# Kernel optimization log

Measured on AMD Instinct MI355X. Metric: run time of the kernel, lower is better.

## Reference

```python
import jax, jax.numpy as jnp
import numpy as np
import math

D_MODEL = 2048
NUM_HEADS = 16
HEAD_DIM = D_MODEL // NUM_HEADS
B, QLEN, CACHE_LEN = 4, 512, 3584

def setup_inputs() -> dict:
    key = jax.random.key(0)
    ks = jax.random.split(key, 13)
    s = 0.02
    return {
        'query': jax.random.normal(ks[0], (B, QLEN, D_MODEL), jnp.float32),
        'key': jax.random.normal(ks[1], (B, QLEN, D_MODEL), jnp.float32),
        'value': jax.random.normal(ks[2], (B, QLEN, D_MODEL), jnp.float32),
        'cached_k': jax.random.normal(ks[3], (B, CACHE_LEN, D_MODEL), jnp.float32),
        'cached_v': jax.random.normal(ks[4], (B, CACHE_LEN, D_MODEL), jnp.float32),
        'wq': jax.random.normal(ks[5], (D_MODEL, D_MODEL), jnp.float32) * s,
        'bq': jnp.zeros((D_MODEL,), jnp.float32),
        'wk': jax.random.normal(ks[6], (D_MODEL, D_MODEL), jnp.float32) * s,
        'bk': jnp.zeros((D_MODEL,), jnp.float32),
        'wv': jax.random.normal(ks[7], (D_MODEL, D_MODEL), jnp.float32) * s,
        'bv': jnp.zeros((D_MODEL,), jnp.float32),
        'wo': jax.random.normal(ks[8], (D_MODEL, D_MODEL), jnp.float32) * s,
        'bo': jnp.zeros((D_MODEL,), jnp.float32),
    }

def _split_heads(x):
    b, s, _ = x.shape
    return x.reshape(b, s, NUM_HEADS, HEAD_DIM).transpose(0, 2, 1, 3)  # [b,h,s,d]

def reference(query, key, value, cached_k, cached_v, wq, bq, wk, bk, wv, bv, wo, bo):
    # projections (torch Linear: x @ W^T + b)
    Q = query @ wq.T + bq
    K_new = key @ wk.T + bk
    V_new = value @ wv.T + bv
    K = jnp.concatenate([cached_k, K_new], axis=1)  # [b, total, d_model]
    V = jnp.concatenate([cached_v, V_new], axis=1)
    seq_len = query.shape[1]
    total_len = K.shape[1]
    cache_len = total_len - seq_len
    Qh = _split_heads(Q)  # [b,h,q,d]
    Kh = _split_heads(K)  # [b,h,t,d]
    Vh = _split_heads(V)
    scale = math.sqrt(HEAD_DIM)
    scores = jnp.einsum('bhqd,bhtd->bhqt', Qh, Kh) / scale
    # causal mask with cache offset: query i attends to keys j <= cache_len + i
    q_idx = jnp.arange(seq_len)[:, None]
    k_idx = jnp.arange(total_len)[None, :]
    mask = k_idx > (q_idx + cache_len)  # True = masked
    scores = jnp.where(mask[None, None], -jnp.inf, scores)
    attn = jax.nn.softmax(scores, axis=-1)
    out = jnp.einsum('bhqt,bhtd->bhqd', attn, Vh)
    out = out.transpose(0, 2, 1, 3).reshape(query.shape[0], seq_len, D_MODEL)
    out = out @ wo.T + bo
    return out
```

## Files before the change

kernel.cpp:

```cpp
#include <hip/hip_runtime.h>

typedef _Float16 half8 __attribute__((ext_vector_type(8)));
typedef _Float16 half4v __attribute__((ext_vector_type(4)));
typedef float f32x4 __attribute__((ext_vector_type(4)));

#define NB 4
#define SQ 512
#define CL 3584
#define TT 4096
#define DM 2048
#define NH 16
#define DH 128

#define KSW(row, col) ((((row) * 128) + (col)) ^ ((((row) & 7) << 3)))
#define VSW(row, col) ((((row) * 64) + (col)) ^ ((((row) & 7) << 3)))
#define PSW(row, col) ((((row) * 64) + (col)) ^ ((((row) & 7) << 3)))

__device__ __forceinline__ void gl_lds16(const void* g, void* l) {
  __builtin_amdgcn_global_load_lds(
      (const __attribute__((address_space(1))) unsigned int*)g,
      (__attribute__((address_space(3))) unsigned int*)l, 16, 0, 0);
}

__global__ __launch_bounds__(256) void cvt_f16(
    const float* __restrict__ s0, const float* __restrict__ s1, const float* __restrict__ s2,
    const float* __restrict__ s3, const float* __restrict__ s4, const float* __restrict__ s5,
    _Float16* __restrict__ d0, _Float16* __restrict__ d1, _Float16* __restrict__ d2,
    _Float16* __restrict__ d3, _Float16* __restrict__ d4, _Float16* __restrict__ d5)
{
  const int z = blockIdx.y;
  const float* s = z == 0 ? s0 : z == 1 ? s1 : z == 2 ? s2 : z == 3 ? s3 : z == 4 ? s4 : s5;
  _Float16* d = z == 0 ? d0 : z == 1 ? d1 : z == 2 ? d2 : z == 3 ? d3 : z == 4 ? d4 : d5;
  const int n4 = DM * DM / 4;
  for (int v = blockIdx.x * blockDim.x + threadIdx.x; v < n4;
       v += gridDim.x * blockDim.x) {
    float4 x = ((const float4*)s)[v];
    half4v h = { (_Float16)x.x, (_Float16)x.y, (_Float16)x.z, (_Float16)x.w };
    ((half4v*)d)[v] = h;
  }
}

__global__ __launch_bounds__(256) void cvt_f16_one(
    const float* __restrict__ s, _Float16* __restrict__ d)
{
  const int n4 = DM * DM / 4;
  for (int v = blockIdx.x * blockDim.x + threadIdx.x; v < n4;
       v += gridDim.x * blockDim.x) {
    float4 x = ((const float4*)s)[v];
    half4v h = { (_Float16)x.x, (_Float16)x.y, (_Float16)x.z, (_Float16)x.w };
    ((half4v*)d)[v] = h;
  }
}

__global__ __launch_bounds__(256) void convert_K(
    const float* __restrict__ ck, _Float16* __restrict__ K)
{
  const long long nvec = (long long)NB * CL * DM / 4;
  const int pb = CL * DM / 4;
  for (long long v = (long long)blockIdx.x * blockDim.x + threadIdx.x; v < nvec;
       v += (long long)gridDim.x * blockDim.x) {
    int b = (int)(v / pb);
    long long r = v - (long long)b * pb;
    float4 x = ((const float4*)ck)[v];
    half4v hx = { (_Float16)x.x, (_Float16)x.y, (_Float16)x.z, (_Float16)x.w };
    ((half4v*)K)[(long long)b * (TT * DM / 4) + r] = hx;
  }
}

__global__ __launch_bounds__(512) void fused_pre(
    const _Float16* __restrict__ A0, const _Float16* __restrict__ A1,
    const _Float16* __restrict__ A2,
    const _Float16* __restrict__ W0, const _Float16* __restrict__ W1,
    const _Float16* __restrict__ W2,
    const float* __restrict__ b0, const float* __restrict__ b1,
    const float* __restrict__ b2,
    _Float16* __restrict__ Qp, _Float16* __restrict__ Kc,
    _Float16* __restrict__ Vt, const float* __restrict__ cv)
{
  __shared__ __align__(16) char smem[4 * 8192];

  const int bid = blockIdx.x;
  const int tid = threadIdx.x;

  if (bid < 768) {
    char* Abuf = smem;
    char* Wbuf = smem + 2 * 8192;
    const int bm = bid & 15, bn = (bid >> 4) & 15, z = bid >> 8;
    const _Float16* Ain = z == 0 ? A0 : z == 1 ? A1 : A2;
    const _Float16* W   = z == 0 ? W0 : z == 1 ? W1 : W2;
    const float* bias   = z == 0 ? b0 : z == 1 ? b1 : b2;

    const int wid = tid >> 6, lane = tid & 63;
    const int wm = wid >> 2, wn = wid & 3;
    const int lr = lane & 15, lg = lane >> 4;

    f32x4 acc[4][2];
#pragma unroll
    for (int i = 0; i < 4; ++i)
#pragma unroll
      for (int j = 0; j < 2; ++j) acc[i][j] = (f32x4){0.f, 0.f, 0.f, 0.f};

    size_t aoff, woff;
    {
      const int o = wid * 1024 + lane * 16;
      const int prow = o >> 7, pb = o & 127;
      const int lb = pb ^ ((prow & 7) << 4);
      const int r = (prow << 1) | (lb >> 6), c = lb & 63;
      aoff = (size_t)(bm * 128 + r) * 4096 + c;
      woff = (size_t)(bn * 128 + r) * 4096 + c;
    }

    auto stage = [&](int kt, int buf) {
      gl_lds16((const char*)Ain + aoff + kt * 64, Abuf + buf * 8192 + wid * 1024);
      gl_lds16((const char*)W + woff + kt * 64, Wbuf + buf * 8192 + wid * 1024);
    };
    auto lds_addr = [](const char* base, int r, int cb) -> const char* {
      return base + ((r >> 1) << 7) + ((((r & 1) << 6) | cb) ^ (((r >> 1) & 7) << 4));
    };
    auto compute = [&](int buf) {
      const char* ab = Abuf + buf * 8192;
      const char* wb = Wbuf + buf * 8192;
      half8 af[4], bf[2];
#pragma unroll
      for (int i = 0; i < 4; ++i)
        af[i] = *(const half8*)lds_addr(ab, wm * 64 + i * 16 + lr, lg << 4);
#pragma unroll
      for (int j = 0; j < 2; ++j)
        bf[j] = *(const half8*)lds_addr(wb, wn * 32 + j * 16 + lr, lg << 4);
#pragma unroll
      for (int i = 0; i < 4; ++i)
#pragma unroll
        for (int j = 0; j < 2; ++j)
          acc[i][j] = __builtin_amdgcn_mfma_f32_16x16x32_f16(af[i], bf[j], acc[i][j], 0, 0, 0);
    };

    const int NKT = DM / 32;
    stage(0, 0);
    __syncthreads();
    for (int kt = 0; kt < NKT; ++kt) {
      if (kt + 1 < NKT) stage(kt + 1, (kt + 1) & 1);
      compute(kt & 1);
      __syncthreads();
    }

    const float qscale = 0.08838834764831845f * 1.4426950408889634f;
#pragma unroll
    for (int i = 0; i < 4; ++i) {
      const int m0 = bm * 128 + wm * 64 + i * 16 + lg * 4;
#pragma unroll
      for (int j = 0; j < 2; ++j) {
        const int gn = bn * 128 + wn * 32 + j * 16 + lr;
        const float bb = bias[gn];
        if (z == 0) {
#pragma unroll
          for (int r = 0; r < 4; ++r)
            Qp[(size_t)(m0 + r) * DM + gn] = (_Float16)((acc[i][j][r] + bb) * qscale);
        } else if (z == 1) {
          const int b = m0 >> 9;
#pragma unroll
          for (int r = 0; r < 4; ++r)
            Kc[((size_t)b * TT + CL + ((m0 + r) & 511)) * DM + gn] =
                (_Float16)(acc[i][j][r] + bb);
        } else {
          half4v hv;
#pragma unroll
          for (int r = 0; r < 4; ++r) hv[r] = (_Float16)(acc[i][j][r] + bb);
          const int b = m0 >> 9, t = CL + (m0 & 511);
          const int h = gn >> 7, d = gn & 127;
          *(half4v*)&Vt[((size_t)(b * NH + h) * DH + d) * TT + t] = hv;
        }
      }
    }
  } else {
    _Float16 (*T)[136] = (_Float16(*)[136])smem;
    const int tv = bid - 768;
    const int b = tv / 896;
    const int rem = tv - b * 896;
    const int t0 = (rem % 56) * 64;
    const int dm0 = (rem / 56) * 128;
    {
      const int tr = tid >> 3, c0 = (tid & 7) * 16;
      const float* src = cv + ((size_t)b * CL + t0 + tr) * DM + dm0 + c0;
      float4 a0 = ((const float4*)src)[0];
      float4 a1 = ((const float4*)src)[1];
      float4 a2 = ((const float4*)src)[2];
      float4 a3 = ((const float4*)src)[3];
      half8 h0 = { (_Float16)a0.x, (_Float16)a0.y, (_Float16)a0.z, (_Float16)a0.w,
                   (_Float16)a1.x, (_Float16)a1.y, (_Float16)a1.z, (_Float16)a1.w };
      half8 h1 = { (_Float16)a2.x, (_Float16)a2.y, (_Float16)a2.z, (_Float16)a2.w,
                   (_Float16)a3.x, (_Float16)a3.y, (_Float16)a3.z, (_Float16)a3.w };
      *(half8*)&T[tr][c0] = h0;
      *(half8*)&T[tr][c0 + 8] = h1;
    }
    __syncthreads();
    {
      const int dl = tid >> 2, tc = (tid & 3) * 16;
      const int h = dm0 >> 7;
      half8 o0, o1;
#pragma unroll
      for (int i = 0; i < 8; ++i) o0[i] = T[tc + i][dl];
#pragma unroll
      for (int i = 0; i < 8; ++i) o1[i] = T[tc + 8 + i][dl];
      _Float16* dst = Vt + ((size_t)(b * NH + h) * DH + dl) * TT + t0 + tc;
      *(half8*)dst = o0;
      *(half8*)(dst + 8) = o1;
    }
  }
}

__global__ __launch_bounds__(512, 4) void mm16o(
    const _Float16* __restrict__ Ain, const _Float16* __restrict__ W,
    const float* __restrict__ bias, float* __restrict__ Co)
{
  __shared__ __align__(16) char smem[4 * 8192];
  char* Abuf = smem;
  char* Wbuf = smem + 2 * 8192;

  const int tid = threadIdx.x;
  const int bm = blockIdx.x, bn = blockIdx.y;
  const int wid = tid >> 6, lane = tid & 63;
  const int wm = wid >> 2, wn = wid & 3;
  const int lr = lane & 15, lg = lane >> 4;

  f32x4 acc[4][2];
#pragma unroll
  for (int i = 0; i < 4; ++i)
#pragma unroll
    for (int j = 0; j < 2; ++j) acc[i][j] = (f32x4){0.f, 0.f, 0.f, 0.f};

  size_t aoff, woff;
  {
    const int o = wid * 1024 + lane * 16;
    const int prow = o >> 7, pb = o & 127;
    const int lb = pb ^ ((prow & 7) << 4);
    const int r = (prow << 1) | (lb >> 6), c = lb & 63;
    aoff = (size_t)(bm * 128 + r) * 4096 + c;
    woff = (size_t)(bn * 128 + r) * 4096 + c;
  }

  auto stage = [&](int kt, int buf) {
    gl_lds16((const char*)Ain + aoff + kt * 64, Abuf + buf * 8192 + wid * 1024);
    gl_lds16((const char*)W + woff + kt * 64, Wbuf + buf * 8192 + wid * 1024);
  };
  auto lds_addr = [](const char* base, int r, int cb) -> const char* {
    return base + ((r >> 1) << 7) + ((((r & 1) << 6) | cb) ^ (((r >> 1) & 7) << 4));
  };
  auto compute = [&](int buf) {
    const char* ab = Abuf + buf * 8192;
    const char* wb = Wbuf + buf * 8192;
    half8 af[4], bf[2];
#pragma unroll
    for (int i = 0; i < 4; ++i)
      af[i] = *(const half8*)lds_addr(ab, wm * 64 + i * 16 + lr, lg << 4);
#pragma unroll
    for (int j = 0; j < 2; ++j)
      bf[j] = *(const half8*)lds_addr(wb, wn * 32 + j * 16 + lr, lg << 4);
#pragma unroll
    for (int i = 0; i < 4; ++i)
#pragma unroll
      for (int j = 0; j < 2; ++j)
        acc[i][j] = __builtin_amdgcn_mfma_f32_16x16x32_f16(af[i], bf[j], acc[i][j], 0, 0, 0);
  };

  const int NKT = DM / 32;
  stage(0, 0);
  __syncthreads();
  for (int kt = 0; kt < NKT; ++kt) {
    if (kt + 1 < NKT) stage(kt + 1, (kt + 1) & 1);
    compute(kt & 1);
    __syncthreads();
  }

#pragma unroll
  for (int i = 0; i < 4; ++i) {
    const int m0 = bm * 128 + wm * 64 + i * 16 + lg * 4;
#pragma unroll
    for (int j = 0; j < 2; ++j) {
      const int gn = bn * 128 + wn * 32 + j * 16 + lr;
      const float bb = bias[gn];
#pragma unroll
      for (int r = 0; r < 4; ++r)
        Co[(size_t)(m0 + r) * DM + gn] = acc[i][j][r] + bb;
    }
  }
}

__global__ __launch_bounds__(512) void attn_kernel(
    const _Float16* __restrict__ Qp, const _Float16* __restrict__ Kc,
    const _Float16* __restrict__ Vt, _Float16* __restrict__ O0,
    _Float16* __restrict__ O1, float2* __restrict__ ml)
{
  __shared__ _Float16 Ks[2][64 * 128];
  __shared__ _Float16 VTs[3][128 * 64];
  __shared__ _Float16 Ps[8][32 * 64];

  const int tid = threadIdx.x;
  const int lin = blockIdx.x;
  const int xcd = lin & 7, slot = lin >> 3;
  const int pair = xcd * 8 + (slot >> 2);
  const int rem = slot & 3;
  const int qb = rem >> 1, part = rem & 1;
  const int b = pair >> 4, h = pair & 15;

  const int wid = tid >> 6, lane = tid & 63;
  const int lr = lane & 15, lg = lane >> 4;
  const int qw = qb * 256 + wid * 32;

  half8 qf[2][4];
#pragma unroll
  for (int qs = 0; qs < 2; ++qs)
#pragma unroll
    for (int kk = 0; kk < 4; ++kk)
      qf[qs][kk] = *(const half8*)&Qp[(size_t)(b * SQ + qw + qs * 16 + lr) * DM +
                                      h * DH + kk * 32 + lg * 8];

  f32x4 zero = {0.f, 0.f, 0.f, 0.f};
  f32x4 acc[8][2];
#pragma unroll
  for (int d = 0; d < 8; ++d)
#pragma unroll
    for (int qs = 0; qs < 2; ++qs) acc[d][qs] = zero;
  float m_run[2] = {-1e30f, -1e30f}, l_run[2] = {0.f, 0.f};

  const int nt_full = (CL + qb * 256 + 256) / 64;
  const int halfn = nt_full >> 1;
  const int tbeg = part ? halfn : 0;
  const int nt = part ? (nt_full - halfn) : halfn;

  int ksrc[2], vsrc[2];
#pragma unroll
  for (int c = 0; c < 2; ++c) {
    const int p = c * 512 + wid * 64 + lane;
    { const int r = p >> 4, pg = p & 15, gc = pg ^ (r & 7);
      ksrc[c] = r * DM + gc * 8; }
    { const int d = p >> 3, pg = p & 7, gt = pg ^ (d & 7);
      vsrc[c] = d * TT + gt * 8; }
  }
  const _Float16* Kb = Kc + (size_t)b * TT * DM + h * DH;
  const _Float16* Vb = Vt + (size_t)(b * NH + h) * DH * TT;

  auto stage = [&](int tt, int kbuf, int vbuf) {
    const int t0 = (tbeg + tt) * 64;
#pragma unroll
    for (int c = 0; c < 2; ++c)
      gl_lds16(Kb + (size_t)t0 * DM + ksrc[c], &Ks[kbuf][(c * 512 + wid * 64) * 8]);
#pragma unroll
    for (int c = 0; c < 2; ++c)
      gl_lds16(Vb + t0 + vsrc[c], &VTs[vbuf][(c * 512 + wid * 64) * 8]);
  };

  auto qk = [&](int kbuf, f32x4 (*s)[2]) {
#pragma unroll
    for (int j = 0; j < 4; ++j)
#pragma unroll
      for (int qs = 0; qs < 2; ++qs) s[j][qs] = zero;
#pragma unroll
    for (int kk = 0; kk < 4; ++kk)
#pragma unroll
      for (int j = 0; j < 4; ++j) {
        half8 kb = *(const half8*)&Ks[kbuf][KSW(j * 16 + lr, kk * 32 + lg * 8)];
        s[j][0] = __builtin_amdgcn_mfma_f32_16x16x32_f16(kb, qf[0][kk], s[j][0], 0, 0, 0);
        s[j][1] = __builtin_amdgcn_mfma_f32_16x16x32_f16(kb, qf[1][kk], s[j][1], 0, 0, 0);
      }
  };

  auto mask_s = [&](int t0, f32x4 (*s)[2]) {
    if (part && t0 + 63 > CL + qw) {
#pragma unroll
      for (int j = 0; j < 4; ++j)
#pragma unroll
        for (int qs = 0; qs < 2; ++qs)
#pragma unroll
          for (int r = 0; r < 4; ++r)
            if (t0 + j * 16 + lg * 4 + r > CL + qw + qs * 16 + lr) s[j][qs][r] = -1e30f;
    }
  };

  auto softmax_step = [&](f32x4 (*s)[2]) {
    float mt[2];
#pragma unroll
    for (int qs = 0; qs < 2; ++qs) {
      float m = s[0][qs][0];
#pragma unroll
      for (int j = 0; j < 4; ++j)
#pragma unroll
        for (int r = 0; r < 4; ++r) m = fmaxf(m, s[j][qs][r]);
      mt[qs] = m;
    }
    if (!__all(mt[0] <= m_run[0] + 10.0f && mt[1] <= m_run[1] + 10.0f)) {
#pragma unroll
      for (int qs = 0; qs < 2; ++qs) {
        float m = fmaxf(mt[qs], __shfl_xor(mt[qs], 16));
        m = fmaxf(m, __shfl_xor(m, 32));
        const float mn = fmaxf(m_run[qs], m);
        const float fsc = exp2f(m_run[qs] - mn);
        m_run[qs] = mn;
        l_run[qs] *= fsc;
#pragma unroll
        for (int d = 0; d < 8; ++d)
#pragma unroll
          for (int r = 0; r < 4; ++r) acc[d][qs][r] *= fsc;
      }
    }
#pragma unroll
    for (int qs = 0; qs < 2; ++qs) {
      float ps = 0.f;
#pragma unroll
      for (int j = 0; j < 4; ++j) {
        float p0 = exp2f(s[j][qs][0] - m_run[qs]);
        float p1 = exp2f(s[j][qs][1] - m_run[qs]);
        float p2 = exp2f(s[j][qs][2] - m_run[qs]);
        float p3 = exp2f(s[j][qs][3] - m_run[qs]);
        ps += (p0 + p1) + (p2 + p3);
        half4v hp = { (_Float16)p0, (_Float16)p1, (_Float16)p2, (_Float16)p3 };
        *(half4v*)&Ps[wid][PSW(qs * 16 + lr, j * 16 + lg * 4)] = hp;
      }
      l_run[qs] += ps;
    }
  };

  auto pv = [&](int vbuf) {
#pragma unroll
    for (int kk = 0; kk < 2; ++kk) {
      half8 pf0 = *(const half8*)&Ps[wid][PSW(lr, kk * 32 + lg * 8)];
      half8 pf1 = *(const half8*)&Ps[wid][PSW(16 + lr, kk * 32 + lg * 8)];
#pragma unroll
      for (int d = 0; d < 8; ++d) {
        half8 vf = *(const half8*)&VTs[vbuf][VSW(d * 16 + lr, kk * 32 + lg * 8)];
        acc[d][0] = __builtin_amdgcn_mfma_f32_16x16x32_f16(vf, pf0, acc[d][0], 0, 0, 0);
        acc[d][1] = __builtin_amdgcn_mfma_f32_16x16x32_f16(vf, pf1, acc[d][1], 0, 0, 0);
      }
    }
  };

  f32x4 sp[4][2], sc[4][2];

  stage(0, 0, 0);
  __syncthreads();
  stage(1, 1, 1);
  qk(0, sp);
  mask_s(tbeg * 64, sp);

  for (int t = 1; t < nt; ++t) {
    __syncthreads();
    if (t + 1 < nt) stage(t + 1, (t + 1) & 1, (t + 1) % 3);
    qk(t & 1, sc);
    softmax_step(sp);
    pv((t - 1) % 3);
    mask_s((tbeg + t) * 64, sc);
#pragma unroll
    for (int j = 0; j < 4; ++j)
#pragma unroll
      for (int qs = 0; qs < 2; ++qs) sp[j][qs] = sc[j][qs];
  }
  softmax_step(sp);
  pv((nt - 1) % 3);

  _Float16* Od = part ? O1 : O0;
#pragma unroll
  for (int qs = 0; qs < 2; ++qs) {
    float lt = l_run[qs] + __shfl_xor(l_run[qs], 16);
    lt += __shfl_xor(lt, 32);
    const float inv = 1.0f / lt;
#pragma unroll
    for (int d = 0; d < 8; ++d) {
      half4v hv;
#pragma unroll
      for (int r = 0; r < 4; ++r) hv[r] = (_Float16)(acc[d][qs][r] * inv);
      *(half4v*)&Od[(size_t)(b * SQ + qw + qs * 16 + lr) * DM + h * DH + d * 16 + lg * 4] = hv;
    }
    if (lg == 0) {
      float2 e; e.x = m_run[qs]; e.y = lt;
      ml[part * (64 * SQ) + ((b * NH + h) * SQ) + qw + qs * 16 + lr] = e;
    }
  }
}

__global__ __launch_bounds__(256) void combine(
    _Float16* __restrict__ AO, const _Float16* __restrict__ O1,
    const float2* __restrict__ ml)
{
  const int idx = blockIdx.x * 256 + threadIdx.x;
  const int row = idx >> 8;
  const int col0 = (idx & 255) * 8;
  const int b = row >> 9, q = row & 511, h = col0 >> 7;
  const float2 e0 = ml[(b * NH + h) * SQ + q];
  const float2 e1 = ml[64 * SQ + (b * NH + h) * SQ + q];
  const float m = fmaxf(e0.x, e1.x);
  float w0 = e0.y * exp2f(e0.x - m);
  float w1 = e1.y * exp2f(e1.x - m);
  const float inv = 1.0f / (w0 + w1);
  w0 *= inv; w1 *= inv;
  const size_t o = (size_t)row * DM + col0;
  half8 a = *(const half8*)&AO[o];
  half8 c = *(const half8*)&O1[o];
  half8 r;
#pragma unroll
  for (int i = 0; i < 8; ++i)
    r[i] = (_Float16)(w0 * (float)a[i] + w1 * (float)c[i]);
  *(half8*)&AO[o] = r;
}

extern "C" void kernel_launch(void* const* d_in, const int* in_sizes, int n_in,
                              void* d_out, int out_size, void* d_ws, size_t ws_size,
                              hipStream_t stream) {
  const float* query = (const float*)d_in[0];
  const float* key   = (const float*)d_in[1];
  const float* value = (const float*)d_in[2];
  const float* ck    = (const float*)d_in[3];
  const float* cv    = (const float*)d_in[4];
  const float* wq = (const float*)d_in[5];
  const float* bq = (const float*)d_in[6];
  const float* wk = (const float*)d_in[7];
  const float* bk = (const float*)d_in[8];
  const float* wv = (const float*)d_in[9];
  const float* bv = (const float*)d_in[10];
  const float* wo = (const float*)d_in[11];
  const float* bo = (const float*)d_in[12];

  char* ws = (char*)d_ws;
  _Float16* Kc = (_Float16*)ws;
  _Float16* Vt = (_Float16*)(ws + 67108864);
  _Float16* Qp = (_Float16*)(ws + 134217728);
  _Float16* AO = (_Float16*)(ws + 142606336);

  _Float16* qh = AO;
  _Float16* kh = (_Float16*)d_out;
  _Float16* vh = (_Float16*)((char*)d_out + 8388608);
  _Float16* wqh = Kc;
  _Float16* wkh = (_Float16*)(ws + 16777216);
  _Float16* wvh = (_Float16*)(ws + 33554432);
  _Float16* woh = Qp;

  _Float16* O1s = (_Float16*)d_out;
  float2* mls = (float2*)((char*)d_out + 8388608);

  cvt_f16<<<dim3(512, 6), 256, 0, stream>>>(
      query, key, value, wq, wk, wv, qh, kh, vh, wqh, wkh, wvh);
  fused_pre<<<768 + 3584, 512, 0, stream>>>(
      qh, kh, vh, wqh, wkh, wvh, bq, bk, bv, Qp, Kc, Vt, cv);
  convert_K<<<2048, 256, 0, stream>>>(ck, Kc);
  attn_kernel<<<256, 512, 0, stream>>>(Qp, Kc, Vt, AO, O1s, mls);
  combine<<<2048, 256, 0, stream>>>(AO, O1s, mls);
  cvt_f16_one<<<512, 256, 0, stream>>>(wo, woh);
  mm16o<<<dim3(16, 16), 512, 0, stream>>>(AO, woh, bo, (float*)d_out);
}
```

Measured before the change: 315.7 us.

## Split attention KV range into four parts with smaller key tiles

Adds an attention kernel that splits each query block's key/value range into four parts instead of two, launching 512 blocks with 32-key tiles, new LDS swizzles and double buffering. A four-way combine kernel merges the partial outputs using the stored max/sum pairs. The aim is better CU occupancy and load balance across the GPU. The cost is extra partial-output traffic, more per-tile synchronisation, and extra workspace; it only runs when the workspace is at least 153 MB, otherwise the old two-way path is used.

```diff
diff --git a/kernel.cpp b/kernel.cpp
--- a/kernel.cpp
+++ b/kernel.cpp
@@ -15,6 +15,8 @@
 #define KSW(row, col) ((((row) * 128) + (col)) ^ ((((row) & 7) << 3)))
 #define VSW(row, col) ((((row) * 64) + (col)) ^ ((((row) & 7) << 3)))
 #define PSW(row, col) ((((row) * 64) + (col)) ^ ((((row) & 7) << 3)))
+#define PSW2(row, col) ((((row) << 5)) + ((col) ^ (((row) & 3) << 3)))
+#define VAD(D, g) ((((D) >> 1) * 64) + ((((((D) & 1) << 2) | (g)) ^ (((D) >> 1) & 7)) << 3))
 
 __device__ __forceinline__ void gl_lds16(const void* g, void* l) {
   __builtin_amdgcn_global_load_lds(
@@ -285,7 +287,214 @@
   }
 }
 
-__global__ __launch_bounds__(512) void attn_kernel(
+__global__ __launch_bounds__(512) void attn_kernel4(
+    const _Float16* __restrict__ Qp, const _Float16* __restrict__ Kc,
+    const _Float16* __restrict__ Vt, _Float16* __restrict__ O0,
+    _Float16* __restrict__ O1, _Float16* __restrict__ O2,
+    _Float16* __restrict__ O3, float2* __restrict__ ml)
+{
+  __shared__ _Float16 Ks[2][32 * 128];
+  __shared__ _Float16 VTs[2][64 * 64];
+  __shared__ _Float16 Ps[8][32 * 32];
+
+  const int tid = threadIdx.x;
+  const int lin = blockIdx.x;
+  const int xcd = lin & 7, slot = lin >> 3;
+  const int pair = xcd * 8 + (slot >> 3);
+  const int rem = slot & 7;
+  const int qb = rem >> 2, part = rem & 3;
+  const int b = pair >> 4, h = pair & 15;
+
+  const int wid = tid >> 6, lane = tid & 63;
+  const int lr = lane & 15, lg = lane >> 4;
+  const int qw = qb * 256 + wid * 32;
+
+  half8 qf[2][4];
+#pragma unroll
+  for (int qs = 0; qs < 2; ++qs)
+#pragma unroll
+    for (int kk = 0; kk < 4; ++kk)
+      qf[qs][kk] = *(const half8*)&Qp[(size_t)(b * SQ + qw + qs * 16 + lr) * DM +
+                                      h * DH + kk * 32 + lg * 8];
+
+  f32x4 zero = {0.f, 0.f, 0.f, 0.f};
+  f32x4 acc[8][2];
+#pragma unroll
+  for (int d = 0; d < 8; ++d)
+#pragma unroll
+    for (int qs = 0; qs < 2; ++qs) acc[d][qs] = zero;
+  float m_run[2] = {-1e30f, -1e30f}, l_run[2] = {0.f, 0.f};
+
+  const int nt_full = (CL + qb * 256 + 256) / 32;
+  const int quarter = nt_full >> 2;
+  const int tbeg = part * quarter;
+  const int nt = quarter;
+
+  int ksrc, vsrc;
+  {
+    const int r = tid >> 4, pg = tid & 15;
+    ksrc = r * DM + (pg ^ (r & 7)) * 8;
+  }
+  {
+    const int line = tid >> 3, slot8 = tid & 7;
+    const int un = slot8 ^ (line & 7);
+    const int d = (line << 1) | (un >> 2), g = un & 3;
+    vsrc = d * TT + g * 8;
+  }
+  const _Float16* Kb = Kc + (size_t)b * TT * DM + h * DH;
+  const _Float16* Vb = Vt + (size_t)(b * NH + h) * DH * TT;
+
+  auto stage = [&](int tt, int buf) {
+    const int t0 = (tbeg + tt) * 32;
+    gl_lds16(Kb + (size_t)t0 * DM + ksrc, &Ks[buf][tid * 8]);
+    gl_lds16(Vb + t0 + vsrc, &VTs[buf][tid * 8]);
+  };
+
+  f32x4 s[2][2];
+
+  stage(0, 0);
+  __syncthreads();
+
+  for (int t = 0; t < nt; ++t) {
+    const int cur = t & 1;
+    if (t + 1 < nt) stage(t + 1, cur ^ 1);
+
+#pragma unroll
+    for (int j = 0; j < 2; ++j)
+#pragma unroll
+      for (int qs = 0; qs < 2; ++qs) s[j][qs] = zero;
+#pragma unroll
+    for (int kk = 0; kk < 4; ++kk)
+#pragma unroll
+      for (int j = 0; j < 2; ++j) {
+        half8 kb = *(const half8*)&Ks[cur][KSW(j * 16 + lr, kk * 32 + lg * 8)];
+        s[j][0] = __builtin_amdgcn_mfma_f32_16x16x32_f16(kb, qf[0][kk], s[j][0], 0, 0, 0);
+        s[j][1] = __builtin_amdgcn_mfma_f32_16x16x32_f16(kb, qf[1][kk], s[j][1], 0, 0, 0);
+      }
+
+    if (part == 3) {
+      const int t0 = (tbeg + t) * 32;
+      if (t0 + 31 > CL + qw) {
+#pragma unroll
+        for (int j = 0; j < 2; ++j)
+#pragma unroll
+          for (int qs = 0; qs < 2; ++qs)
+#pragma unroll
+            for (int r = 0; r < 4; ++r)
+              if (t0 + j * 16 + lg * 4 + r > CL + qw + qs * 16 + lr) s[j][qs][r] = -1e30f;
+      }
+    }
+
+    float mt[2];
+#pragma unroll
+    for (int qs = 0; qs < 2; ++qs) {
+      float m = s[0][qs][0];
+#pragma unroll
+      for (int j = 0; j < 2; ++j)
+#pragma unroll
+        for (int r = 0; r < 4; ++r) m = fmaxf(m, s[j][qs][r]);
+      mt[qs] = m;
+    }
+    if (!__all(mt[0] <= m_run[0] + 10.0f && mt[1] <= m_run[1] + 10.0f)) {
+#pragma unroll
+      for (int qs = 0; qs < 2; ++qs) {
+        float m = fmaxf(mt[qs], __shfl_xor(mt[qs], 16));
+        m = fmaxf(m, __shfl_xor(m, 32));
+        const float mn = fmaxf(m_run[qs], m);
+        const float fsc = exp2f(m_run[qs] - mn);
+        m_run[qs] = mn;
+        l_run[qs] *= fsc;
+#pragma unroll
+        for (int d = 0; d < 8; ++d)
+#pragma unroll
+          for (int r = 0; r < 4; ++r) acc[d][qs][r] *= fsc;
+      }
+    }
+#pragma unroll
+    for (int qs = 0; qs < 2; ++qs) {
+      float ps = 0.f;
+#pragma unroll
+      for (int j = 0; j < 2; ++j) {
+        float p0 = exp2f(s[j][qs][0] - m_run[qs]);
+        float p1 = exp2f(s[j][qs][1] - m_run[qs]);
+        float p2 = exp2f(s[j][qs][2] - m_run[qs]);
+        float p3 = exp2f(s[j][qs][3] - m_run[qs]);
+        ps += (p0 + p1) + (p2 + p3);
+        half4v hp = { (_Float16)p0, (_Float16)p1, (_Float16)p2, (_Float16)p3 };
+        *(half4v*)&Ps[wid][PSW2(qs * 16 + lr, j * 16 + lg * 4)] = hp;
+      }
+      l_run[qs] += ps;
+    }
+
+    {
+      half8 pf0 = *(const half8*)&Ps[wid][PSW2(lr, lg * 8)];
+      half8 pf1 = *(const half8*)&Ps[wid][PSW2(16 + lr, lg * 8)];
+#pragma unroll
+      for (int d = 0; d < 8; ++d) {
+        half8 vf = *(const half8*)&VTs[cur][VAD(d * 16 + lr, lg)];
+        acc[d][0] = __builtin_amdgcn_mfma_f32_16x16x32_f16(vf, pf0, acc[d][0], 0, 0, 0);
+        acc[d][1] = __builtin_amdgcn_mfma_f32_16x16x32_f16(vf, pf1, acc[d][1], 0, 0, 0);
+      }
+    }
+
+    __syncthreads();
+  }
+
+  _Float16* Od = part == 0 ? O0 : part == 1 ? O1 : part == 2 ? O2 : O3;
+#pragma unroll
+  for (int qs = 0; qs < 2; ++qs) {
+    float lt = l_run[qs] + __shfl_xor(l_run[qs], 16);
+    lt += __shfl_xor(lt, 32);
+    const float inv = 1.0f / lt;
+#pragma unroll
+    for (int d = 0; d < 8; ++d) {
+      half4v hv;
+#pragma unroll
+      for (int r = 0; r < 4; ++r) hv[r] = (_Float16)(acc[d][qs][r] * inv);
+      *(half4v*)&Od[(size_t)(b * SQ + qw + qs * 16 + lr) * DM + h * DH + d * 16 + lg * 4] = hv;
+    }
+    if (lg == 0) {
+      float2 e; e.x = m_run[qs]; e.y = lt;
+      ml[part * (64 * SQ) + ((b * NH + h) * SQ) + qw + qs * 16 + lr] = e;
+    }
+  }
+}
+
+__global__ __launch_bounds__(256) void combine4(
+    _Float16* __restrict__ AO, const _Float16* __restrict__ O1,
+    const _Float16* __restrict__ O2, const _Float16* __restrict__ O3,
+    const float2* __restrict__ ml)
+{
+  const int idx = blockIdx.x * 256 + threadIdx.x;
+  const int row = idx >> 8;
+  const int col0 = (idx & 255) * 8;
+  const int b = row >> 9, q = row & 511, h = col0 >> 7;
+  const int base = (b * NH + h) * SQ + q;
+  float2 e0 = ml[base];
+  float2 e1 = ml[64 * SQ + base];
+  float2 e2 = ml[2 * 64 * SQ + base];
+  float2 e3 = ml[3 * 64 * SQ + base];
+  float m = fmaxf(fmaxf(e0.x, e1.x), fmaxf(e2.x, e3.x));
+  float w0 = e0.y * exp2f(e0.x - m);
+  float w1 = e1.y * exp2f(e1.x - m);
+  float w2 = e2.y * exp2f(e2.x - m);
+  float w3 = e3.y * exp2f(e3.x - m);
+  const float inv = 1.0f / (((w0 + w1) + (w2 + w3)));
+  w0 *= inv; w1 *= inv; w2 *= inv; w3 *= inv;
+  const size_t o = (size_t)row * DM + col0;
+  half8 a = *(const half8*)&AO[o];
+  half8 c1 = *(const half8*)&O1[o];
+  half8 c2 = *(const half8*)&O2[o];
+  half8 c3 = *(const half8*)&O3[o];
+  half8 r;
+#pragma unroll
+  for (int i = 0; i < 8; ++i)
+    r[i] = (_Float16)(w0 * (float)a[i] + w1 * (float)c1[i] +
+                      w2 * (float)c2[i] + w3 * (float)c3[i]);
+  *(half8*)&AO[o] = r;
+}
+
+__global__ __launch_bounds__(512) void attn_kernel2(
     const _Float16* __restrict__ Qp, const _Float16* __restrict__ Kc,
     const _Float16* __restrict__ Vt, _Float16* __restrict__ O0,
     _Float16* __restrict__ O1, float2* __restrict__ ml)
@@ -476,7 +685,7 @@
   }
 }
 
-__global__ __launch_bounds__(256) void combine(
+__global__ __launch_bounds__(256) void combine2(
     _Float16* __restrict__ AO, const _Float16* __restrict__ O1,
     const float2* __restrict__ ml)
 {
@@ -532,16 +741,27 @@
   _Float16* wvh = (_Float16*)(ws + 33554432);
   _Float16* woh = Qp;
 
-  _Float16* O1s = (_Float16*)d_out;
-  float2* mls = (float2*)((char*)d_out + 8388608);
-
   cvt_f16<<<dim3(512, 6), 256, 0, stream>>>(
       query, key, value, wq, wk, wv, qh, kh, vh, wqh, wkh, wvh);
   fused_pre<<<768 + 3584, 512, 0, stream>>>(
       qh, kh, vh, wqh, wkh, wvh, bq, bk, bv, Qp, Kc, Vt, cv);
   convert_K<<<2048, 256, 0, stream>>>(ck, Kc);
-  attn_kernel<<<256, 512, 0, stream>>>(Qp, Kc, Vt, AO, O1s, mls);
-  combine<<<2048, 256, 0, stream>>>(AO, O1s, mls);
+
+  const bool big = ws_size >= (size_t)153 * 1024 * 1024;
+  if (big) {
+    _Float16* O1s = (_Float16*)d_out;
+    _Float16* O2s = (_Float16*)((char*)d_out + 8388608);
+    _Float16* O3s = (_Float16*)(ws + 150994944);
+    float2* mls = (float2*)(ws + 159383552);
+    attn_kernel4<<<512, 512, 0, stream>>>(Qp, Kc, Vt, AO, O1s, O2s, O3s, mls);
+    combine4<<<2048, 256, 0, stream>>>(AO, O1s, O2s, O3s, mls);
+  } else {
+    _Float16* O1s = (_Float16*)d_out;
+    float2* mls = (float2*)((char*)d_out + 8388608);
+    attn_kernel2<<<256, 512, 0, stream>>>(Qp, Kc, Vt, AO, O1s, mls);
+    combine2<<<2048, 256, 0, stream>>>(AO, O1s, mls);
+  }
+
   cvt_f16_one<<<512, 256, 0, stream>>>(wo, woh);
   mm16o<<<dim3(16, 16), 512, 0, stream>>>(AO, woh, bo, (float*)d_out);
 }
```

Result: slower. 338.9 us (+7.3%).

## Fuse fp32 weight conversion into QKV GEMM staging and fold K-cache conversion

Applied to the files above, without the earlier changes.

The QKV projection GEMM now reads fp32 weights directly. It converts them to fp16 in registers with packed round-toward-zero conversion and writes them to LDS itself, so the separate pass that converted the three weight matrices is gone. The cached-K conversion kernel is folded into fused_pre as 1024 extra blocks, which removes one launch and lets that work overlap with the GEMM and V-transpose blocks. In exchange, each weight tile is fetched as fp32 by every M-block, doubling the weight bytes read from cache. The W staging also now goes through registers rather than direct global-to-LDS loads, and round-toward-zero changes the weight rounding slightly.

```diff
diff --git a/kernel.cpp b/kernel.cpp
--- a/kernel.cpp
+++ b/kernel.cpp
@@ -24,13 +24,11 @@
 
 __global__ __launch_bounds__(256) void cvt_f16(
     const float* __restrict__ s0, const float* __restrict__ s1, const float* __restrict__ s2,
-    const float* __restrict__ s3, const float* __restrict__ s4, const float* __restrict__ s5,
-    _Float16* __restrict__ d0, _Float16* __restrict__ d1, _Float16* __restrict__ d2,
-    _Float16* __restrict__ d3, _Float16* __restrict__ d4, _Float16* __restrict__ d5)
+    _Float16* __restrict__ d0, _Float16* __restrict__ d1, _Float16* __restrict__ d2)
 {
   const int z = blockIdx.y;
-  const float* s = z == 0 ? s0 : z == 1 ? s1 : z == 2 ? s2 : z == 3 ? s3 : z == 4 ? s4 : s5;
-  _Float16* d = z == 0 ? d0 : z == 1 ? d1 : z == 2 ? d2 : z == 3 ? d3 : z == 4 ? d4 : d5;
+  const float* s = z == 0 ? s0 : z == 1 ? s1 : s2;
+  _Float16* d = z == 0 ? d0 : z == 1 ? d1 : d2;
   const int n4 = DM * DM / 4;
   for (int v = blockIdx.x * blockDim.x + threadIdx.x; v < n4;
        v += gridDim.x * blockDim.x) {
@@ -52,30 +50,16 @@
   }
 }
 
-__global__ __launch_bounds__(256) void convert_K(
-    const float* __restrict__ ck, _Float16* __restrict__ K)
-{
-  const long long nvec = (long long)NB * CL * DM / 4;
-  const int pb = CL * DM / 4;
-  for (long long v = (long long)blockIdx.x * blockDim.x + threadIdx.x; v < nvec;
-       v += (long long)gridDim.x * blockDim.x) {
-    int b = (int)(v / pb);
-    long long r = v - (long long)b * pb;
-    float4 x = ((const float4*)ck)[v];
-    half4v hx = { (_Float16)x.x, (_Float16)x.y, (_Float16)x.z, (_Float16)x.w };
-    ((half4v*)K)[(long long)b * (TT * DM / 4) + r] = hx;
-  }
-}
-
 __global__ __launch_bounds__(512) void fused_pre(
     const _Float16* __restrict__ A0, const _Float16* __restrict__ A1,
     const _Float16* __restrict__ A2,
-    const _Float16* __restrict__ W0, const _Float16* __restrict__ W1,
-    const _Float16* __restrict__ W2,
+    const float* __restrict__ Wq, const float* __restrict__ Wk,
+    const float* __restrict__ Wv,
     const float* __restrict__ b0, const float* __restrict__ b1,
     const float* __restrict__ b2,
     _Float16* __restrict__ Qp, _Float16* __restrict__ Kc,
-    _Float16* __restrict__ Vt, const float* __restrict__ cv)
+    _Float16* __restrict__ Vt, const float* __restrict__ cv,
+    const float* __restrict__ ck)
 {
   __shared__ __align__(16) char smem[4 * 8192];
 
@@ -87,7 +71,7 @@
     char* Wbuf = smem + 2 * 8192;
     const int bm = bid & 15, bn = (bid >> 4) & 15, z = bid >> 8;
     const _Float16* Ain = z == 0 ? A0 : z == 1 ? A1 : A2;
-    const _Float16* W   = z == 0 ? W0 : z == 1 ? W1 : W2;
+    const float* Wf     = z == 0 ? Wq : z == 1 ? Wk : Wv;
     const float* bias   = z == 0 ? b0 : z == 1 ? b1 : b2;
 
     const int wid = tid >> 6, lane = tid & 63;
@@ -100,19 +84,31 @@
 #pragma unroll
       for (int j = 0; j < 2; ++j) acc[i][j] = (f32x4){0.f, 0.f, 0.f, 0.f};
 
-    size_t aoff, woff;
+    size_t aoff, woff32;
     {
       const int o = wid * 1024 + lane * 16;
       const int prow = o >> 7, pb = o & 127;
       const int lb = pb ^ ((prow & 7) << 4);
       const int r = (prow << 1) | (lb >> 6), c = lb & 63;
       aoff = (size_t)(bm * 128 + r) * 4096 + c;
-      woff = (size_t)(bn * 128 + r) * 4096 + c;
-    }
-
-    auto stage = [&](int kt, int buf) {
-      gl_lds16((const char*)Ain + aoff + kt * 64, Abuf + buf * 8192 + wid * 1024);
-      gl_lds16((const char*)W + woff + kt * 64, Wbuf + buf * 8192 + wid * 1024);
+      woff32 = (size_t)(bn * 128 + r) * 8192 + (size_t)c * 2;
+    }
+    const int ldst = wid * 1024 + lane * 16;
+
+    float4 wr0, wr1;
+    auto stage_load = [&](int kt) {
+      gl_lds16((const char*)Ain + aoff + kt * 64, Abuf + ((kt & 1) * 8192) + ldst);
+      const char* wp = (const char*)Wf + woff32 + (size_t)kt * 128;
+      wr0 = *(const float4*)wp;
+      wr1 = *(const float4*)(wp + 16);
+    };
+    auto stage_write = [&](int buf) {
+      int u0 = __builtin_bit_cast(int, __builtin_amdgcn_cvt_pkrtz(wr0.x, wr0.y));
+      int u1 = __builtin_bit_cast(int, __builtin_amdgcn_cvt_pkrtz(wr0.z, wr0.w));
+      int u2 = __builtin_bit_cast(int, __builtin_amdgcn_cvt_pkrtz(wr1.x, wr1.y));
+      int u3 = __builtin_bit_cast(int, __builtin_amdgcn_cvt_pkrtz(wr1.z, wr1.w));
+      uint4 u = { (unsigned)u0, (unsigned)u1, (unsigned)u2, (unsigned)u3 };
+      *(uint4*)(Wbuf + buf * 8192 + ldst) = u;
     };
     auto lds_addr = [](const char* base, int r, int cb) -> const char* {
       return base + ((r >> 1) << 7) + ((((r & 1) << 6) | cb) ^ (((r >> 1) & 7) << 4));
@@ -135,11 +131,13 @@
     };
 
     const int NKT = DM / 32;
-    stage(0, 0);
+    stage_load(0);
+    stage_write(0);
     __syncthreads();
     for (int kt = 0; kt < NKT; ++kt) {
-      if (kt + 1 < NKT) stage(kt + 1, (kt + 1) & 1);
+      if (kt + 1 < NKT) stage_load(kt + 1);
       compute(kt & 1);
+      if (kt + 1 < NKT) stage_write((kt + 1) & 1);
       __syncthreads();
     }
 
@@ -171,7 +169,7 @@
         }
       }
     }
-  } else {
+  } else if (bid < 768 + 3584) {
     _Float16 (*T)[136] = (_Float16(*)[136])smem;
     const int tv = bid - 768;
     const int b = tv / 896;
@@ -205,6 +203,18 @@
       *(half8*)dst = o0;
       *(half8*)(dst + 8) = o1;
     }
+  } else {
+    const int cb = bid - (768 + 3584);
+    const long long nvec = (long long)NB * CL * DM / 4;
+    const int pb = CL * DM / 4;
+    const long long stride = 1024LL * 512;
+    for (long long v = (long long)cb * 512 + tid; v < nvec; v += stride) {
+      int b = (int)(v / pb);
+      long long r = v - (long long)b * pb;
+      float4 x = ((const float4*)ck)[v];
+      half4v hx = { (_Float16)x.x, (_Float16)x.y, (_Float16)x.z, (_Float16)x.w };
+      ((half4v*)Kc)[(long long)b * (TT * DM / 4) + r] = hx;
+    }
   }
 }
 
@@ -239,8 +249,8 @@
   }
 
   auto stage = [&](int kt, int buf) {
-    gl_lds16((const char*)Ain + aoff + kt * 64, Abuf + buf * 8192 + wid * 1024);
-    gl_lds16((const char*)W + woff + kt * 64, Wbuf + buf * 8192 + wid * 1024);
+    gl_lds16((const char*)Ain + aoff + kt * 64, Abuf + buf * 8192 + wid * 1024 + (tid & 63) * 16);
+    gl_lds16((const char*)W + woff + kt * 64, Wbuf + buf * 8192 + wid * 1024 + (tid & 63) * 16);
   };
   auto lds_addr = [](const char* base, int r, int cb) -> const char* {
     return base + ((r >> 1) << 7) + ((((r & 1) << 6) | cb) ^ (((r >> 1) & 7) << 4));
@@ -527,19 +537,14 @@
   _Float16* qh = AO;
   _Float16* kh = (_Float16*)d_out;
   _Float16* vh = (_Float16*)((char*)d_out + 8388608);
-  _Float16* wqh = Kc;
-  _Float16* wkh = (_Float16*)(ws + 16777216);
-  _Float16* wvh = (_Float16*)(ws + 33554432);
   _Float16* woh = Qp;
 
   _Float16* O1s = (_Float16*)d_out;
   float2* mls = (float2*)((char*)d_out + 8388608);
 
-  cvt_f16<<<dim3(512, 6), 256, 0, stream>>>(
-      query, key, value, wq, wk, wv, qh, kh, vh, wqh, wkh, wvh);
-  fused_pre<<<768 + 3584, 512, 0, stream>>>(
-      qh, kh, vh, wqh, wkh, wvh, bq, bk, bv, Qp, Kc, Vt, cv);
-  convert_K<<<2048, 256, 0, stream>>>(ck, Kc);
+  cvt_f16<<<dim3(512, 3), 256, 0, stream>>>(query, key, value, qh, kh, vh);
+  fused_pre<<<768 + 3584 + 1024, 512, 0, stream>>>(
+      qh, kh, vh, wq, wk, wv, bq, bk, bv, Qp, Kc, Vt, cv, ck);
   attn_kernel<<<256, 512, 0, stream>>>(Qp, Kc, Vt, AO, O1s, mls);
   combine<<<2048, 256, 0, stream>>>(AO, O1s, mls);
   cvt_f16_one<<<512, 256, 0, stream>>>(wo, woh);
```

Result: slower. 332.5 us (+5.3%).

## Fold half of cached-K conversion into fused_pre and unroll attention loop by two

Applied to the files above, without the earlier changes.

When the workspace is large enough, the fp16 weight copies are moved so that batches 2-3 of cached_k can be converted by extra blocks inside fused_pre, running alongside the projection GEMM and V transpose. The standalone conversion kernel then handles only batches 0-1. The attention main loop is unrolled by two with ping-pong score buffers to remove the per-iteration register copy and the conditional stage. The change also assumes both attention parts have equal tile counts (nt = halfn), which only holds when nt_full is even, and it adds a workspace-size dependency for the new layout.

```diff
diff --git a/kernel.cpp b/kernel.cpp
--- a/kernel.cpp
+++ b/kernel.cpp
@@ -52,12 +52,11 @@
   }
 }
 
-__global__ __launch_bounds__(256) void convert_K(
-    const float* __restrict__ ck, _Float16* __restrict__ K)
-{
-  const long long nvec = (long long)NB * CL * DM / 4;
+__global__ __launch_bounds__(256) void convert_Kpart(
+    const float* __restrict__ ck, _Float16* __restrict__ K, long long v0, long long v1)
+{
   const int pb = CL * DM / 4;
-  for (long long v = (long long)blockIdx.x * blockDim.x + threadIdx.x; v < nvec;
+  for (long long v = v0 + (long long)blockIdx.x * blockDim.x + threadIdx.x; v < v1;
        v += (long long)gridDim.x * blockDim.x) {
     int b = (int)(v / pb);
     long long r = v - (long long)b * pb;
@@ -75,7 +74,8 @@
     const float* __restrict__ b0, const float* __restrict__ b1,
     const float* __restrict__ b2,
     _Float16* __restrict__ Qp, _Float16* __restrict__ Kc,
-    _Float16* __restrict__ Vt, const float* __restrict__ cv)
+    _Float16* __restrict__ Vt, const float* __restrict__ cv,
+    const float* __restrict__ ck)
 {
   __shared__ __align__(16) char smem[4 * 8192];
 
@@ -171,7 +171,7 @@
         }
       }
     }
-  } else {
+  } else if (bid < 768 + 3584) {
     _Float16 (*T)[136] = (_Float16(*)[136])smem;
     const int tv = bid - 768;
     const int b = tv / 896;
@@ -205,6 +205,19 @@
       *(half8*)dst = o0;
       *(half8*)(dst + 8) = o1;
     }
+  } else {
+    const int cb = bid - (768 + 3584);
+    const int pb = CL * DM / 4;
+    const long long nvec = (long long)NB * pb;
+    const long long vhalf = 2LL * pb;
+    const long long stride = 1024LL * 512;
+    for (long long v = vhalf + (long long)cb * 512 + tid; v < nvec; v += stride) {
+      int b = (int)(v / pb);
+      long long r = v - (long long)b * pb;
+      float4 x = ((const float4*)ck)[v];
+      half4v hx = { (_Float16)x.x, (_Float16)x.y, (_Float16)x.z, (_Float16)x.w };
+      ((half4v*)Kc)[(long long)b * (TT * DM / 4) + r] = hx;
+    }
   }
 }
 
@@ -325,7 +338,7 @@
   const int nt_full = (CL + qb * 256 + 256) / 64;
   const int halfn = nt_full >> 1;
   const int tbeg = part ? halfn : 0;
-  const int nt = part ? (nt_full - halfn) : halfn;
+  const int nt = halfn;
 
   int ksrc[2], vsrc[2];
 #pragma unroll
@@ -433,28 +446,37 @@
     }
   };
 
-  f32x4 sp[4][2], sc[4][2];
+  f32x4 sA[4][2], sB[4][2];
 
   stage(0, 0, 0);
   __syncthreads();
   stage(1, 1, 1);
-  qk(0, sp);
-  mask_s(tbeg * 64, sp);
-
-  for (int t = 1; t < nt; ++t) {
+  qk(0, sA);
+  mask_s(tbeg * 64, sA);
+
+  int t = 1;
+  for (; t + 1 < nt; t += 2) {
     __syncthreads();
-    if (t + 1 < nt) stage(t + 1, (t + 1) & 1, (t + 1) % 3);
-    qk(t & 1, sc);
-    softmax_step(sp);
+    stage(t + 1, (t + 1) & 1, (t + 1) % 3);
+    qk(t & 1, sB);
+    softmax_step(sA);
     pv((t - 1) % 3);
-    mask_s((tbeg + t) * 64, sc);
-#pragma unroll
-    for (int j = 0; j < 4; ++j)
-#pragma unroll
-      for (int qs = 0; qs < 2; ++qs) sp[j][qs] = sc[j][qs];
-  }
-  softmax_step(sp);
-  pv((nt - 1) % 3);
+    mask_s((tbeg + t) * 64, sB);
+
+    __syncthreads();
+    stage(t + 2, (t + 2) & 1, (t + 2) % 3);
+    qk((t + 1) & 1, sA);
+    softmax_step(sB);
+    pv(t % 3);
+    mask_s((tbeg + t + 1) * 64, sA);
+  }
+  __syncthreads();
+  qk(t & 1, sB);
+  softmax_step(sA);
+  pv((t - 1) % 3);
+  mask_s((tbeg + t) * 64, sB);
+  softmax_step(sB);
+  pv(t % 3);
 
   _Float16* Od = part ? O1 : O0;
 #pragma unroll
@@ -527,19 +549,34 @@
   _Float16* qh = AO;
   _Float16* kh = (_Float16*)d_out;
   _Float16* vh = (_Float16*)((char*)d_out + 8388608);
-  _Float16* wqh = Kc;
-  _Float16* wkh = (_Float16*)(ws + 16777216);
-  _Float16* wvh = (_Float16*)(ws + 33554432);
   _Float16* woh = Qp;
 
   _Float16* O1s = (_Float16*)d_out;
   float2* mls = (float2*)((char*)d_out + 8388608);
 
-  cvt_f16<<<dim3(512, 6), 256, 0, stream>>>(
-      query, key, value, wq, wk, wv, qh, kh, vh, wqh, wkh, wvh);
-  fused_pre<<<768 + 3584, 512, 0, stream>>>(
-      qh, kh, vh, wqh, wkh, wvh, bq, bk, bv, Qp, Kc, Vt, cv);
-  convert_K<<<2048, 256, 0, stream>>>(ck, Kc);
+  const long long pb4 = (long long)CL * DM / 4;
+  const bool big = ws_size >= (size_t)153 * 1024 * 1024;
+
+  if (big) {
+    _Float16* wqh = (_Float16*)(ws + 150994944);
+    _Float16* wkh = Kc;
+    _Float16* wvh = Kc + (size_t)TT * DM;
+    cvt_f16<<<dim3(512, 6), 256, 0, stream>>>(
+        query, key, value, wq, wk, wv, qh, kh, vh, wqh, wkh, wvh);
+    fused_pre<<<768 + 3584 + 1024, 512, 0, stream>>>(
+        qh, kh, vh, wqh, wkh, wvh, bq, bk, bv, Qp, Kc, Vt, cv, ck);
+    convert_Kpart<<<1024, 256, 0, stream>>>(ck, Kc, 0, 2 * pb4);
+  } else {
+    _Float16* wqh = Kc;
+    _Float16* wkh = (_Float16*)(ws + 16777216);
+    _Float16* wvh = (_Float16*)(ws + 33554432);
+    cvt_f16<<<dim3(512, 6), 256, 0, stream>>>(
+        query, key, value, wq, wk, wv, qh, kh, vh, wqh, wkh, wvh);
+    fused_pre<<<768 + 3584, 512, 0, stream>>>(
+        qh, kh, vh, wqh, wkh, wvh, bq, bk, bv, Qp, Kc, Vt, cv, ck);
+    convert_Kpart<<<2048, 256, 0, stream>>>(ck, Kc, 0, 4 * pb4);
+  }
+
   attn_kernel<<<256, 512, 0, stream>>>(Qp, Kc, Vt, AO, O1s, mls);
   combine<<<2048, 256, 0, stream>>>(AO, O1s, mls);
   cvt_f16_one<<<512, 256, 0, stream>>>(wo, woh);
```

Result: slower. 357.5 us (+13.2%).
